# Kernel optimization log

Measured on AMD Instinct MI355X. Metric: run time of the kernel, lower is better.

Reference implementation:

```python
import jax, jax.numpy as jnp
import numpy as np

B, LQ, LK, D, H = 2, 1024, 1024, 1024, 16
DH = D // H


def setup_inputs() -> dict:
    key = jax.random.key(0)
    ks = jax.random.split(key, 14)
    s = 1.0 / np.sqrt(D)
    inp = {
        "q": jax.random.normal(ks[0], (B, LQ, D), jnp.float32),
        "k": jax.random.normal(ks[1], (B, LK, D), jnp.float32),
        "v": jax.random.normal(ks[2], (B, LK, D), jnp.float32),
        "Wq": jax.random.normal(ks[3], (D, D), jnp.float32) * s,
        "bq": jnp.zeros((D,), jnp.float32),
        "Wk": jax.random.normal(ks[4], (D, D), jnp.float32) * s,
        "bk": jnp.zeros((D,), jnp.float32),
        "Wv": jax.random.normal(ks[5], (D, D), jnp.float32) * s,
        "bv": jnp.zeros((D,), jnp.float32),
        "Wo": jax.random.normal(ks[6], (D, D), jnp.float32) * s,
        "bo": jnp.zeros((D,), jnp.float32),
        "logits_bias": jax.random.normal(ks[7], (B, LQ, LK), jnp.float32),
        "key_padding_mask": jax.random.randint(ks[8], (B, LK), 0, 2) > 0,
    }
    return inp


def _split_heads(x):
    b, l, _ = x.shape
    return x.reshape(b, l, H, DH).transpose(0, 2, 1, 3)  # [B,H,L,DH]


def reference(q, k, v, Wq, bq, Wk, bk, Wv, bv, Wo, bo, logits_bias, key_padding_mask):
    qh = _split_heads(q @ Wq.T + bq)  # [B,H,Lq,DH]
    kh = _split_heads(k @ Wk.T + bk)  # [B,H,Lk,DH]
    vh = _split_heads(v @ Wv.T + bv)  # [B,H,Lk,DH]

    neg = jnp.finfo(qh.dtype).min
    # attn_mask = logits_bias broadcast over heads, masked_fill at padded keys
    attn_mask = jnp.where(key_padding_mask[:, None, None, :],
                          neg, logits_bias[:, None, :, :])  # [B,1,Lq,Lk]

    scale = 1.0 / np.sqrt(DH)
    scores = jnp.einsum('bhqd,bhkd->bhqk', qh, kh) * scale + attn_mask
    probs = jax.nn.softmax(scores, axis=-1)
    out = jnp.einsum('bhqk,bhkd->bhqd', probs, vh)  # [B,H,Lq,DH]
    out = out.transpose(0, 2, 1, 3).reshape(q.shape[0], q.shape[1], D)
    return out @ Wo.T + bo
```

## Files before the change

### kernel.cpp

```cpp
#include <hip/hip_runtime.h>


typedef _Float16 half8 __attribute__((ext_vector_type(8)));
typedef float f32x4 __attribute__((ext_vector_type(4)));

#define MFMA16(a, b, c) __builtin_amdgcn_mfma_f32_16x16x32_f16((a), (b), (c), 0, 0, 0)

__device__ __forceinline__ void gload16(const void* g, void* l) {
  __builtin_amdgcn_global_load_lds(
      (const __attribute__((address_space(1))) unsigned int*)g,
      (__attribute__((address_space(3))) unsigned int*)l, 16, 0, 0);
}

__device__ __forceinline__ half8 frag_ld(const _Float16* t, int row, int ck) {
  return *(const half8*)(t + row * 64 + (((ck ^ (row & 7)) << 3)));
}

__global__ __launch_bounds__(256) void cvt_f32_f16(
    const float* __restrict__ q, const float* __restrict__ k, const float* __restrict__ v,
    _Float16* __restrict__ q16, _Float16* __restrict__ k16, _Float16* __restrict__ v16) {
  const float* s;
  _Float16* d;
  if (blockIdx.y == 0) { s = q; d = q16; }
  else if (blockIdx.y == 1) { s = k; d = k16; }
  else { s = v; d = v16; }
  const size_t i = ((size_t)blockIdx.x * 256 + threadIdx.x) * 8;
  const float4 a = *(const float4*)(s + i);
  const float4 b = *(const float4*)(s + i + 4);
  half8 h;
  h[0] = (_Float16)a.x; h[1] = (_Float16)a.y; h[2] = (_Float16)a.z; h[3] = (_Float16)a.w;
  h[4] = (_Float16)b.x; h[5] = (_Float16)b.y; h[6] = (_Float16)b.z; h[7] = (_Float16)b.w;
  *(half8*)(d + i) = h;
}

__global__ __launch_bounds__(256) void mm_bt(
    const _Float16* __restrict__ Aq, const _Float16* __restrict__ Ak,
    const _Float16* __restrict__ Av, const float* __restrict__ W0,
    const float* __restrict__ W1, const float* __restrict__ W2,
    const float* __restrict__ c0, const float* __restrict__ c1,
    const float* __restrict__ c2, _Float16* __restrict__ Dq,
    _Float16* __restrict__ Dk, _Float16* __restrict__ Dvt,
    float* __restrict__ Df, int is_final) {
  __shared__ __align__(16) _Float16 lds[17408];
  _Float16* As = lds;
  _Float16* Bs = lds + 8192;

  const int tid = threadIdx.x;
  const int wv = tid >> 6, ln = tid & 63;
  const int quad = ln >> 4, col = ln & 15;
  const int wm = wv >> 1, wn = wv & 1;
  const int n0 = blockIdx.x * 128;
  const int m0 = blockIdx.y * 128;
  const int z = blockIdx.z;

  const _Float16* A = (z == 0) ? Aq : (z == 1) ? Ak : Av;
  const float* Bw = (z == 0) ? W0 : (z == 1) ? W1 : W2;
  const float* bias = (z == 0) ? c0 : (z == 1) ? c1 : c2;

  const f32x4 zero4 = {0.f, 0.f, 0.f, 0.f};
  f32x4 acc[4][4];
#pragma unroll
  for (int i = 0; i < 4; ++i)
#pragma unroll
    for (int j = 0; j < 4; ++j) acc[i][j] = zero4;

  for (int k0 = 0; k0 < 1024; k0 += 64) {
    __syncthreads();
#pragma unroll
    for (int j = 0; j < 4; ++j) {
      const int ci = j * 256 + wv * 64 + ln;
      const int row = ci >> 3;
      const int lc = (ci & 7) ^ (row & 7);
      gload16(A + (size_t)(m0 + row) * 1024 + k0 + lc * 8,
              As + (size_t)(j * 256 + wv * 64) * 8);
    }
#pragma unroll
    for (int j = 0; j < 4; ++j) {
      const int ci = j * 256 + tid;
      const int row = ci >> 3;
      const int lc = (ci & 7) ^ (row & 7);
      const float* sp = Bw + (size_t)(n0 + row) * 1024 + k0 + lc * 8;
      const float4 u = *(const float4*)sp;
      const float4 w = *(const float4*)(sp + 4);
      half8 h;
      h[0] = (_Float16)u.x; h[1] = (_Float16)u.y; h[2] = (_Float16)u.z; h[3] = (_Float16)u.w;
      h[4] = (_Float16)w.x; h[5] = (_Float16)w.y; h[6] = (_Float16)w.z; h[7] = (_Float16)w.w;
      *(half8*)(Bs + (size_t)ci * 8) = h;
    }
    __syncthreads();
#pragma unroll
    for (int kk = 0; kk < 2; ++kk) {
      half8 af[4], bf[4];
#pragma unroll
      for (int mi = 0; mi < 4; ++mi)
        af[mi] = frag_ld(As, wm * 64 + mi * 16 + col, kk * 4 + quad);
#pragma unroll
      for (int ni = 0; ni < 4; ++ni)
        bf[ni] = frag_ld(Bs, wn * 64 + ni * 16 + col, kk * 4 + quad);
#pragma unroll
      for (int mi = 0; mi < 4; ++mi)
#pragma unroll
        for (int ni = 0; ni < 4; ++ni)
          acc[mi][ni] = MFMA16(af[mi], bf[ni], acc[mi][ni]);
    }
  }

  float bv[4];
#pragma unroll
  for (int ni = 0; ni < 4; ++ni) bv[ni] = bias[n0 + wn * 64 + ni * 16 + col];

  if (is_final) {
#pragma unroll
    for (int mi = 0; mi < 4; ++mi) {
      const int m_g = m0 + wm * 64 + mi * 16 + quad * 4;
#pragma unroll
      for (int ni = 0; ni < 4; ++ni) {
        const int n_g = n0 + wn * 64 + ni * 16 + col;
#pragma unroll
        for (int r = 0; r < 4; ++r)
          Df[(size_t)(m_g + r) * 1024 + n_g] = acc[mi][ni][r] + bv[ni];
      }
    }
  } else if (z < 2) {
    _Float16* D = z ? Dk : Dq;
#pragma unroll
    for (int mi = 0; mi < 4; ++mi) {
      const int m_g = m0 + wm * 64 + mi * 16 + quad * 4;
#pragma unroll
      for (int ni = 0; ni < 4; ++ni) {
        const int n_g = n0 + wn * 64 + ni * 16 + col;
        const int h = n_g >> 6, dh = n_g & 63;
#pragma unroll
        for (int r = 0; r < 4; ++r) {
          const int b = (m_g + r) >> 10, l = (m_g + r) & 1023;
          D[((size_t)((b * 16 + h) * 1024) + l) * 64 + dh] =
              (_Float16)(acc[mi][ni][r] + bv[ni]);
        }
      }
    }
  } else {
    __syncthreads();
    _Float16* Ct = lds;
#pragma unroll
    for (int mi = 0; mi < 4; ++mi) {
      const int ml = wm * 64 + mi * 16 + quad * 4;
#pragma unroll
      for (int ni = 0; ni < 4; ++ni) {
        const int nl = wn * 64 + ni * 16 + col;
#pragma unroll
        for (int r = 0; r < 4; ++r)
          Ct[(size_t)nl * 136 + ml + r] = (_Float16)(acc[mi][ni][r] + bv[ni]);
      }
    }
    __syncthreads();
#pragma unroll
    for (int it = 0; it < 8; ++it) {
      const int ci = it * 256 + tid;
      const int n = ci >> 4;
      const int mc = (ci & 15) * 8;
      const half8 hv = *(const half8*)(Ct + (size_t)n * 136 + mc);
      const int n_g = n0 + n;
      const int h = n_g >> 6, dh = n_g & 63;
      const int m_g = m0 + mc;
      const int b = m_g >> 10, l = m_g & 1023;
      *(half8*)(Dvt + ((size_t)((b * 16 + h) * 64 + dh)) * 1024 + l) = hv;
    }
  }
}

__global__ __launch_bounds__(256) void attn(
    const _Float16* __restrict__ Qh, const _Float16* __restrict__ Kh,
    const _Float16* __restrict__ Vt, const float* __restrict__ biasL,
    const int* __restrict__ kpm, _Float16* __restrict__ AO) {
  __shared__ __align__(16) _Float16 Qs[4096];
  __shared__ __align__(16) _Float16 Ks[4096];
  __shared__ __align__(16) _Float16 Vs[4096];
  __shared__ __align__(16) _Float16 Ps[4][1024];

  const int tid = threadIdx.x;
  const int wv = tid >> 6, ln = tid & 63;
  const int quad = ln >> 4, col = ln & 15;
  const int q0 = blockIdx.x * 64;
  const int bh = blockIdx.y;
  const int b = bh >> 4, hh = bh & 15;
  const int qrow_base = q0 + wv * 16 + quad * 4;

#pragma unroll
  for (int j = 0; j < 2; ++j) {
    const int ci = j * 256 + wv * 64 + ln;
    const int row = ci >> 3;
    const int lc = (ci & 7) ^ (row & 7);
    gload16(Qh + ((size_t)bh * 1024 + q0 + row) * 64 + lc * 8,
            Qs + (size_t)(j * 256 + wv * 64) * 8);
  }

  const f32x4 zero4 = {0.f, 0.f, 0.f, 0.f};
  f32x4 o[4];
#pragma unroll
  for (int ni = 0; ni < 4; ++ni) o[ni] = zero4;
  float m_i[4] = {-1e30f, -1e30f, -1e30f, -1e30f};
  float l_i[4] = {0.f, 0.f, 0.f, 0.f};

  for (int k0 = 0; k0 < 1024; k0 += 64) {
    __syncthreads();
#pragma unroll
    for (int j = 0; j < 2; ++j) {
      const int ci = j * 256 + wv * 64 + ln;
      const int row = ci >> 3;
      const int lc = (ci & 7) ^ (row & 7);
      gload16(Kh + ((size_t)bh * 1024 + k0 + row) * 64 + lc * 8,
              Ks + (size_t)(j * 256 + wv * 64) * 8);
      gload16(Vt + ((size_t)(bh * 64 + row)) * 1024 + k0 + lc * 8,
              Vs + (size_t)(j * 256 + wv * 64) * 8);
    }
    float bb[4][4];
    int mk[4];
#pragma unroll
    for (int ni = 0; ni < 4; ++ni) {
      const int kg = k0 + ni * 16 + col;
      mk[ni] = kpm[b * 1024 + kg];
#pragma unroll
      for (int r = 0; r < 4; ++r)
        bb[ni][r] = biasL[((size_t)(b * 1024 + qrow_base + r)) * 1024 + kg];
    }
    __syncthreads();

    const half8 aq0 = frag_ld(Qs, wv * 16 + col, quad);
    const half8 aq1 = frag_ld(Qs, wv * 16 + col, 4 + quad);
    f32x4 s[4];
#pragma unroll
    for (int ni = 0; ni < 4; ++ni) {
      f32x4 z4 = zero4;
      const half8 b0 = frag_ld(Ks, ni * 16 + col, quad);
      const half8 b1 = frag_ld(Ks, ni * 16 + col, 4 + quad);
      z4 = MFMA16(aq0, b0, z4);
      z4 = MFMA16(aq1, b1, z4);
      s[ni] = z4;
    }

#pragma unroll
    for (int ni = 0; ni < 4; ++ni)
#pragma unroll
      for (int r = 0; r < 4; ++r)
        s[ni][r] = mk[ni] ? -1e9f : (s[ni][r] * 0.125f + bb[ni][r]);

    float alpha[4];
#pragma unroll
    for (int r = 0; r < 4; ++r) {
      float rm = fmaxf(fmaxf(s[0][r], s[1][r]), fmaxf(s[2][r], s[3][r]));
#pragma unroll
      for (int off = 1; off < 16; off <<= 1) rm = fmaxf(rm, __shfl_xor(rm, off, 16));
      const float mn = fmaxf(m_i[r], rm);
      alpha[r] = __expf(m_i[r] - mn);
      m_i[r] = mn;
      float ps = 0.f;
#pragma unroll
      for (int ni = 0; ni < 4; ++ni) {
        const float p = __expf(s[ni][r] - mn);
        s[ni][r] = p;
        ps += p;
      }
#pragma unroll
      for (int off = 1; off < 16; off <<= 1) ps += __shfl_xor(ps, off, 16);
      l_i[r] = l_i[r] * alpha[r] + ps;
    }
#pragma unroll
    for (int ni = 0; ni < 4; ++ni)
#pragma unroll
      for (int r = 0; r < 4; ++r) o[ni][r] *= alpha[r];

    _Float16* Pw = Ps[wv];
#pragma unroll
    for (int ni = 0; ni < 4; ++ni)
#pragma unroll
      for (int r = 0; r < 4; ++r) {
        const int row = quad * 4 + r;
        const int k = ni * 16 + col;
        Pw[row * 64 + ((((k >> 3) ^ (row & 7)) << 3) | (k & 7))] = (_Float16)s[ni][r];
      }
    __syncthreads();

    const half8 ap0 = frag_ld(Pw, col, quad);
    const half8 ap1 = frag_ld(Pw, col, 4 + quad);
#pragma unroll
    for (int ni = 0; ni < 4; ++ni) {
      const half8 b0 = frag_ld(Vs, ni * 16 + col, quad);
      const half8 b1 = frag_ld(Vs, ni * 16 + col, 4 + quad);
      o[ni] = MFMA16(ap0, b0, o[ni]);
      o[ni] = MFMA16(ap1, b1, o[ni]);
    }
  }

#pragma unroll
  for (int r = 0; r < 4; ++r) {
    const float inv = 1.0f / l_i[r];
    const int qg = qrow_base + r;
#pragma unroll
    for (int ni = 0; ni < 4; ++ni) {
      const int dh = ni * 16 + col;
      AO[((size_t)(b * 1024 + qg)) * 1024 + hh * 64 + dh] = (_Float16)(o[ni][r] * inv);
    }
  }
}

extern "C" void kernel_launch(void* const* d_in, const int* in_sizes, int n_in,
                              void* d_out, int out_size, void* d_ws, size_t ws_size,
                              hipStream_t stream) {
  (void)in_sizes; (void)n_in; (void)out_size; (void)ws_size;
  const float* q = (const float*)d_in[0];
  const float* k = (const float*)d_in[1];
  const float* v = (const float*)d_in[2];
  const float* Wq = (const float*)d_in[3];
  const float* bq = (const float*)d_in[4];
  const float* Wk = (const float*)d_in[5];
  const float* bk = (const float*)d_in[6];
  const float* Wv = (const float*)d_in[7];
  const float* bv = (const float*)d_in[8];
  const float* Wo = (const float*)d_in[9];
  const float* bo = (const float*)d_in[10];
  const float* lb = (const float*)d_in[11];
  const int* kpm = (const int*)d_in[12];
  float* out = (float*)d_out;

  const size_t NT = (size_t)2 * 1024 * 1024;
  _Float16* q16 = (_Float16*)d_ws;
  _Float16* k16 = q16 + NT;
  _Float16* v16 = k16 + NT;
  _Float16* Qh = v16 + NT;
  _Float16* Kh = Qh + NT;
  _Float16* Vt = Kh + NT;
  _Float16* AO = q16;

  cvt_f32_f16<<<dim3(1024, 3), 256, 0, stream>>>(q, k, v, q16, k16, v16);
  mm_bt<<<dim3(8, 16, 3), 256, 0, stream>>>(q16, k16, v16, Wq, Wk, Wv, bq, bk, bv,
                                            Qh, Kh, Vt, nullptr, 0);
  attn<<<dim3(16, 32), 256, 0, stream>>>(Qh, Kh, Vt, lb, kpm, AO);
  mm_bt<<<dim3(8, 16, 1), 256, 0, stream>>>(AO, nullptr, nullptr, Wo, nullptr, nullptr,
                                            bo, nullptr, nullptr, nullptr, nullptr,
                                            nullptr, out, 1);
}
```

Measured before the change: 200.7 us.

## Pre-convert weights to fp16 and transpose attention score layout per query column

The weight matrices are converted to fp16 once in the conversion kernel, so the projection GEMM can load them with async global-to-LDS copies instead of per-tile fp32 loads and in-register conversion. The attention kernel swaps the MFMA operands so that each lane owns a single query row. This turns the bias and mask reads into vector loads, cuts the row reductions to two cross-quad shuffles, and drops a block-wide barrier before the P·V step. The cost is an extra conversion pass over the weights each call and more workspace.

New measurement: 185.6 us. 7.5% less time.

```diff
diff --git a/kernel.cpp b/kernel.cpp
--- a/kernel.cpp
+++ b/kernel.cpp
@@ -2,6 +2,7 @@
 
 
 typedef _Float16 half8 __attribute__((ext_vector_type(8)));
+typedef _Float16 half4_t __attribute__((ext_vector_type(4)));
 typedef float f32x4 __attribute__((ext_vector_type(4)));
 
 #define MFMA16(a, b, c) __builtin_amdgcn_mfma_f32_16x16x32_f16((a), (b), (c), 0, 0, 0)
@@ -18,25 +19,36 @@
 
 __global__ __launch_bounds__(256) void cvt_f32_f16(
     const float* __restrict__ q, const float* __restrict__ k, const float* __restrict__ v,
-    _Float16* __restrict__ q16, _Float16* __restrict__ k16, _Float16* __restrict__ v16) {
+    const float* __restrict__ Wq, const float* __restrict__ Wk,
+    const float* __restrict__ Wv, const float* __restrict__ Wo,
+    _Float16* __restrict__ q16, _Float16* __restrict__ k16, _Float16* __restrict__ v16,
+    _Float16* __restrict__ w16) {
+  const int y = blockIdx.y;
+  if (y >= 3 && blockIdx.x >= 512) return;
   const float* s;
   _Float16* d;
-  if (blockIdx.y == 0) { s = q; d = q16; }
-  else if (blockIdx.y == 1) { s = k; d = k16; }
-  else { s = v; d = v16; }
+  const size_t M = (size_t)1024 * 1024;
+  switch (y) {
+    case 0: s = q;  d = q16; break;
+    case 1: s = k;  d = k16; break;
+    case 2: s = v;  d = v16; break;
+    case 3: s = Wq; d = w16; break;
+    case 4: s = Wk; d = w16 + M; break;
+    case 5: s = Wv; d = w16 + 2 * M; break;
+    default: s = Wo; d = w16 + 3 * M; break;
+  }
   const size_t i = ((size_t)blockIdx.x * 256 + threadIdx.x) * 8;
   const float4 a = *(const float4*)(s + i);
-  const float4 b = *(const float4*)(s + i + 4);
+  const float4 bvv = *(const float4*)(s + i + 4);
   half8 h;
   h[0] = (_Float16)a.x; h[1] = (_Float16)a.y; h[2] = (_Float16)a.z; h[3] = (_Float16)a.w;
-  h[4] = (_Float16)b.x; h[5] = (_Float16)b.y; h[6] = (_Float16)b.z; h[7] = (_Float16)b.w;
+  h[4] = (_Float16)bvv.x; h[5] = (_Float16)bvv.y; h[6] = (_Float16)bvv.z; h[7] = (_Float16)bvv.w;
   *(half8*)(d + i) = h;
 }
 
 __global__ __launch_bounds__(256) void mm_bt(
     const _Float16* __restrict__ Aq, const _Float16* __restrict__ Ak,
-    const _Float16* __restrict__ Av, const float* __restrict__ W0,
-    const float* __restrict__ W1, const float* __restrict__ W2,
+    const _Float16* __restrict__ Av, const _Float16* __restrict__ W16,
     const float* __restrict__ c0, const float* __restrict__ c1,
     const float* __restrict__ c2, _Float16* __restrict__ Dq,
     _Float16* __restrict__ Dk, _Float16* __restrict__ Dvt,
@@ -54,7 +66,7 @@
   const int z = blockIdx.z;
 
   const _Float16* A = (z == 0) ? Aq : (z == 1) ? Ak : Av;
-  const float* Bw = (z == 0) ? W0 : (z == 1) ? W1 : W2;
+  const _Float16* Bw = W16 + (size_t)z * 1024 * 1024;
   const float* bias = (z == 0) ? c0 : (z == 1) ? c1 : c2;
 
   const f32x4 zero4 = {0.f, 0.f, 0.f, 0.f};
@@ -73,19 +85,8 @@
       const int lc = (ci & 7) ^ (row & 7);
       gload16(A + (size_t)(m0 + row) * 1024 + k0 + lc * 8,
               As + (size_t)(j * 256 + wv * 64) * 8);
-    }
-#pragma unroll
-    for (int j = 0; j < 4; ++j) {
-      const int ci = j * 256 + tid;
-      const int row = ci >> 3;
-      const int lc = (ci & 7) ^ (row & 7);
-      const float* sp = Bw + (size_t)(n0 + row) * 1024 + k0 + lc * 8;
-      const float4 u = *(const float4*)sp;
-      const float4 w = *(const float4*)(sp + 4);
-      half8 h;
-      h[0] = (_Float16)u.x; h[1] = (_Float16)u.y; h[2] = (_Float16)u.z; h[3] = (_Float16)u.w;
-      h[4] = (_Float16)w.x; h[5] = (_Float16)w.y; h[6] = (_Float16)w.z; h[7] = (_Float16)w.w;
-      *(half8*)(Bs + (size_t)ci * 8) = h;
+      gload16(Bw + (size_t)(n0 + row) * 1024 + k0 + lc * 8,
+              Bs + (size_t)(j * 256 + wv * 64) * 8);
     }
     __syncthreads();
 #pragma unroll
@@ -175,7 +176,7 @@
   __shared__ __align__(16) _Float16 Qs[4096];
   __shared__ __align__(16) _Float16 Ks[4096];
   __shared__ __align__(16) _Float16 Vs[4096];
-  __shared__ __align__(16) _Float16 Ps[4][1024];
+  __shared__ __align__(16) _Float16 Pt[4096];
 
   const int tid = threadIdx.x;
   const int wv = tid >> 6, ln = tid & 63;
@@ -183,7 +184,7 @@
   const int q0 = blockIdx.x * 64;
   const int bh = blockIdx.y;
   const int b = bh >> 4, hh = bh & 15;
-  const int qrow_base = q0 + wv * 16 + quad * 4;
+  const int qg = q0 + wv * 16 + col;
 
 #pragma unroll
   for (int j = 0; j < 2; ++j) {
@@ -193,13 +194,17 @@
     gload16(Qh + ((size_t)bh * 1024 + q0 + row) * 64 + lc * 8,
             Qs + (size_t)(j * 256 + wv * 64) * 8);
   }
+  __syncthreads();
+  const half8 bq0 = frag_ld(Qs, wv * 16 + col, quad);
+  const half8 bq1 = frag_ld(Qs, wv * 16 + col, 4 + quad);
 
   const f32x4 zero4 = {0.f, 0.f, 0.f, 0.f};
   f32x4 o[4];
 #pragma unroll
   for (int ni = 0; ni < 4; ++ni) o[ni] = zero4;
-  float m_i[4] = {-1e30f, -1e30f, -1e30f, -1e30f};
-  float l_i[4] = {0.f, 0.f, 0.f, 0.f};
+  float m_i = -1e30f, l_i = 0.f;
+
+  _Float16* Pw = Pt + wv * 1024;
 
   for (int k0 = 0; k0 < 1024; k0 += 64) {
     __syncthreads();
@@ -213,93 +218,85 @@
       gload16(Vt + ((size_t)(bh * 64 + row)) * 1024 + k0 + lc * 8,
               Vs + (size_t)(j * 256 + wv * 64) * 8);
     }
-    float bb[4][4];
-    int mk[4];
-#pragma unroll
-    for (int ni = 0; ni < 4; ++ni) {
-      const int kg = k0 + ni * 16 + col;
-      mk[ni] = kpm[b * 1024 + kg];
+    f32x4 bb[4];
+    int4 mk4[4];
+#pragma unroll
+    for (int mi = 0; mi < 4; ++mi) {
+      const int kg = k0 + mi * 16 + quad * 4;
+      mk4[mi] = *(const int4*)&kpm[b * 1024 + kg];
+      bb[mi] = *(const f32x4*)&biasL[((size_t)(b * 1024 + qg)) * 1024 + kg];
+    }
+    __syncthreads();
+
+    f32x4 s[4];
+#pragma unroll
+    for (int mi = 0; mi < 4; ++mi) {
+      f32x4 a4 = zero4;
+      a4 = MFMA16(frag_ld(Ks, mi * 16 + col, quad), bq0, a4);
+      a4 = MFMA16(frag_ld(Ks, mi * 16 + col, 4 + quad), bq1, a4);
+      s[mi] = a4;
+    }
+#pragma unroll
+    for (int mi = 0; mi < 4; ++mi) {
+      const int* mp = (const int*)&mk4[mi];
 #pragma unroll
       for (int r = 0; r < 4; ++r)
-        bb[ni][r] = biasL[((size_t)(b * 1024 + qrow_base + r)) * 1024 + kg];
-    }
-    __syncthreads();
-
-    const half8 aq0 = frag_ld(Qs, wv * 16 + col, quad);
-    const half8 aq1 = frag_ld(Qs, wv * 16 + col, 4 + quad);
-    f32x4 s[4];
-#pragma unroll
-    for (int ni = 0; ni < 4; ++ni) {
-      f32x4 z4 = zero4;
-      const half8 b0 = frag_ld(Ks, ni * 16 + col, quad);
-      const half8 b1 = frag_ld(Ks, ni * 16 + col, 4 + quad);
-      z4 = MFMA16(aq0, b0, z4);
-      z4 = MFMA16(aq1, b1, z4);
-      s[ni] = z4;
-    }
-
-#pragma unroll
-    for (int ni = 0; ni < 4; ++ni)
-#pragma unroll
-      for (int r = 0; r < 4; ++r)
-        s[ni][r] = mk[ni] ? -1e9f : (s[ni][r] * 0.125f + bb[ni][r]);
-
-    float alpha[4];
-#pragma unroll
-    for (int r = 0; r < 4; ++r) {
-      float rm = fmaxf(fmaxf(s[0][r], s[1][r]), fmaxf(s[2][r], s[3][r]));
-#pragma unroll
-      for (int off = 1; off < 16; off <<= 1) rm = fmaxf(rm, __shfl_xor(rm, off, 16));
-      const float mn = fmaxf(m_i[r], rm);
-      alpha[r] = __expf(m_i[r] - mn);
-      m_i[r] = mn;
-      float ps = 0.f;
-#pragma unroll
-      for (int ni = 0; ni < 4; ++ni) {
-        const float p = __expf(s[ni][r] - mn);
-        s[ni][r] = p;
+        s[mi][r] = mp[r] ? -1e9f : s[mi][r] * 0.125f + bb[mi][r];
+    }
+
+    float rm = -1e30f;
+#pragma unroll
+    for (int mi = 0; mi < 4; ++mi)
+#pragma unroll
+      for (int r = 0; r < 4; ++r) rm = fmaxf(rm, s[mi][r]);
+    rm = fmaxf(rm, __shfl_xor(rm, 16));
+    rm = fmaxf(rm, __shfl_xor(rm, 32));
+    const float mn = fmaxf(m_i, rm);
+    const float alpha = __expf(m_i - mn);
+    m_i = mn;
+    float ps = 0.f;
+#pragma unroll
+    for (int mi = 0; mi < 4; ++mi)
+#pragma unroll
+      for (int r = 0; r < 4; ++r) {
+        const float p = __expf(s[mi][r] - mn);
+        s[mi][r] = p;
         ps += p;
       }
-#pragma unroll
-      for (int off = 1; off < 16; off <<= 1) ps += __shfl_xor(ps, off, 16);
-      l_i[r] = l_i[r] * alpha[r] + ps;
-    }
+    ps += __shfl_xor(ps, 16);
+    ps += __shfl_xor(ps, 32);
+    l_i = l_i * alpha + ps;
 #pragma unroll
     for (int ni = 0; ni < 4; ++ni)
 #pragma unroll
-      for (int r = 0; r < 4; ++r) o[ni][r] *= alpha[r];
-
-    _Float16* Pw = Ps[wv];
-#pragma unroll
-    for (int ni = 0; ni < 4; ++ni)
-#pragma unroll
-      for (int r = 0; r < 4; ++r) {
-        const int row = quad * 4 + r;
-        const int k = ni * 16 + col;
-        Pw[row * 64 + ((((k >> 3) ^ (row & 7)) << 3) | (k & 7))] = (_Float16)s[ni][r];
-      }
-    __syncthreads();
-
-    const half8 ap0 = frag_ld(Pw, col, quad);
-    const half8 ap1 = frag_ld(Pw, col, 4 + quad);
+      for (int r = 0; r < 4; ++r) o[ni][r] *= alpha;
+
+#pragma unroll
+    for (int mi = 0; mi < 4; ++mi) {
+      half4_t h;
+      h[0] = (_Float16)s[mi][0]; h[1] = (_Float16)s[mi][1];
+      h[2] = (_Float16)s[mi][2]; h[3] = (_Float16)s[mi][3];
+      const int kloc = mi * 16 + quad * 4;
+      const int chunk = kloc >> 3;
+      *(half4_t*)(Pw + col * 64 + (((chunk ^ (col & 7)) << 3) | (kloc & 7))) = h;
+    }
+    const half8 p0 = frag_ld(Pw, col, quad);
+    const half8 p1 = frag_ld(Pw, col, 4 + quad);
+
 #pragma unroll
     for (int ni = 0; ni < 4; ++ni) {
-      const half8 b0 = frag_ld(Vs, ni * 16 + col, quad);
-      const half8 b1 = frag_ld(Vs, ni * 16 + col, 4 + quad);
-      o[ni] = MFMA16(ap0, b0, o[ni]);
-      o[ni] = MFMA16(ap1, b1, o[ni]);
-    }
-  }
-
-#pragma unroll
-  for (int r = 0; r < 4; ++r) {
-    const float inv = 1.0f / l_i[r];
-    const int qg = qrow_base + r;
-#pragma unroll
-    for (int ni = 0; ni < 4; ++ni) {
-      const int dh = ni * 16 + col;
-      AO[((size_t)(b * 1024 + qg)) * 1024 + hh * 64 + dh] = (_Float16)(o[ni][r] * inv);
-    }
+      o[ni] = MFMA16(frag_ld(Vs, ni * 16 + col, quad), p0, o[ni]);
+      o[ni] = MFMA16(frag_ld(Vs, ni * 16 + col, 4 + quad), p1, o[ni]);
+    }
+  }
+
+  const float inv = 1.0f / l_i;
+#pragma unroll
+  for (int ni = 0; ni < 4; ++ni) {
+    half4_t h;
+#pragma unroll
+    for (int r = 0; r < 4; ++r) h[r] = (_Float16)(o[ni][r] * inv);
+    *(half4_t*)&AO[((size_t)(b * 1024 + qg)) * 1024 + hh * 64 + ni * 16 + quad * 4] = h;
   }
 }
 
@@ -329,13 +326,15 @@
   _Float16* Qh = v16 + NT;
   _Float16* Kh = Qh + NT;
   _Float16* Vt = Kh + NT;
+  _Float16* w16 = Vt + NT;
   _Float16* AO = q16;
 
-  cvt_f32_f16<<<dim3(1024, 3), 256, 0, stream>>>(q, k, v, q16, k16, v16);
-  mm_bt<<<dim3(8, 16, 3), 256, 0, stream>>>(q16, k16, v16, Wq, Wk, Wv, bq, bk, bv,
+  cvt_f32_f16<<<dim3(1024, 7), 256, 0, stream>>>(q, k, v, Wq, Wk, Wv, Wo,
+                                                 q16, k16, v16, w16);
+  mm_bt<<<dim3(8, 16, 3), 256, 0, stream>>>(q16, k16, v16, w16, bq, bk, bv,
                                             Qh, Kh, Vt, nullptr, 0);
   attn<<<dim3(16, 32), 256, 0, stream>>>(Qh, Kh, Vt, lb, kpm, AO);
-  mm_bt<<<dim3(8, 16, 1), 256, 0, stream>>>(AO, nullptr, nullptr, Wo, nullptr, nullptr,
+  mm_bt<<<dim3(8, 16, 1), 256, 0, stream>>>(AO, nullptr, nullptr, w16 + 3 * NT / 2,
                                             bo, nullptr, nullptr, nullptr, nullptr,
                                             nullptr, out, 1);
 }
```
